# Performance work log

Hardware: AMD Instinct MI355X
Metric: run time of the kernel (lower is better)

## Reference

```python
import jax, jax.numpy as jnp
import numpy as np

MAX_LEN = 960
EMB = 200
SQRT_DK = np.sqrt(MAX_LEN).astype(np.float32)  # note: sqrt(max_len), as in source


def setup_inputs() -> dict:
    key = jax.random.key(0)
    k1, k2, k3, k4 = jax.random.split(key, 4)
    B, S, F = 16, 2048, 800
    x = jax.random.normal(k1, (B, S, F), dtype=jnp.float32)
    # torch Linear(960,200) weight init scale ~ 1/sqrt(960); random normal scaled
    scale = 1.0 / np.sqrt(MAX_LEN)
    Wq = jax.random.normal(k2, (MAX_LEN, EMB), dtype=jnp.float32) * scale
    Wk = jax.random.normal(k3, (MAX_LEN, EMB), dtype=jnp.float32) * scale
    Wv = jax.random.normal(k4, (MAX_LEN, EMB), dtype=jnp.float32) * scale
    return {"x": x, "Wq": Wq, "Wk": Wk, "Wv": Wv}


def reference(x, Wq, Wk, Wv):
    # pad feature dim up to MAX_LEN with zeros
    pad = MAX_LEN - x.shape[2]
    x = jnp.pad(x, ((0, 0), (0, 0), (0, pad)))
    gelu = lambda t: jax.nn.gelu(t, approximate=False)  # torch nn.GELU default = exact
    q = gelu(jnp.einsum('bsf,fe->bse', x, Wq))  # [B,S,E]
    k = gelu(jnp.einsum('bsf,fe->bse', x, Wk))
    v = gelu(jnp.einsum('bsf,fe->bse', x, Wv))
    score = jnp.einsum('bqe,bke->bqk', q, k) / SQRT_DK  # [B,S,S]
    attn = jax.nn.softmax(score, axis=-1)
    return jnp.einsum('bqk,bke->bqe', attn, v)  # [B,S,E]
```

## Files before the change

### kernel.cpp

```cpp
#include <hip/hip_runtime.h>
#include <hip/hip_bf16.h>

#define B_  16
#define S_  2048
#define F_  800
#define E_  200
#define EP  224
#define KP  832
#define KSP 256
#define M_  (B_ * S_)

typedef __attribute__((ext_vector_type(8))) short short8;
typedef __attribute__((ext_vector_type(4))) float f32x4;

#define QSCL (0.03227486121839514f * 1.4426950408889634f)

__device__ __forceinline__ unsigned short f2bf(float f) {
    __hip_bfloat16 h = __float2bfloat16(f);
    return *reinterpret_cast<unsigned short*>(&h);
}

__device__ __forceinline__ float exp2_fast(float x) {
    float r;
    asm("v_exp_f32 %0, %1" : "=v"(r) : "v"(x));
    return r;
}

__device__ __forceinline__ float rcp_fast(float x) {
    float r;
    asm("v_rcp_f32 %0, %1" : "=v"(r) : "v"(x));
    return r;
}

__device__ __forceinline__ float gelu_fast(float x) {
    const float i = x + 0.044715f * x * x * x;
    const float z = 2.302265314f * i;
    return x * rcp_fast(1.0f + exp2_fast(-z));
}

__device__ __forceinline__ void gload_lds16(const void* g, void* l) {
    __builtin_amdgcn_global_load_lds(
        (const __attribute__((address_space(1))) unsigned int*)g,
        (__attribute__((address_space(3))) unsigned int*)l, 16, 0, 0);
}

__global__ __launch_bounds__(256)
void prep_x(const float* __restrict__ x, unsigned short* __restrict__ xb) {
    const int id = blockIdx.x * 256 + threadIdx.x;
    const int r  = id / (KP / 8);
    const int c8 = id % (KP / 8);
    ushort4 lo = {0, 0, 0, 0}, hi = {0, 0, 0, 0};
    if (c8 < F_ / 8) {
        const float4 a = *reinterpret_cast<const float4*>(x + (size_t)r * F_ + c8 * 8);
        const float4 b = *reinterpret_cast<const float4*>(x + (size_t)r * F_ + c8 * 8 + 4);
        lo.x = f2bf(a.x); lo.y = f2bf(a.y); lo.z = f2bf(a.z); lo.w = f2bf(a.w);
        hi.x = f2bf(b.x); hi.y = f2bf(b.y); hi.z = f2bf(b.z); hi.w = f2bf(b.w);
    }
    unsigned short* dst = xb + (size_t)r * KP + c8 * 8;
    *reinterpret_cast<ushort4*>(dst) = lo;
    *reinterpret_cast<ushort4*>(dst + 4) = hi;
}

__global__ __launch_bounds__(256)
void prep_w(const float* __restrict__ Wq, const float* __restrict__ Wk,
            const float* __restrict__ Wv, unsigned short* __restrict__ wt) {
    const int id = blockIdx.x * 256 + threadIdx.x;
    const int sel = id / (EP * KP);
    const int rem = id % (EP * KP);
    const int e = rem / KP;
    const int k = rem % KP;
    const float* W = (sel == 0) ? Wq : ((sel == 1) ? Wk : Wv);
    float v = (e < E_ && k < F_) ? W[(size_t)k * E_ + e] : 0.0f;
    wt[id] = f2bf(v);
}

#define STAGE(XB, WB, KK) do {                                                   \
    const int k0s = (KK) * 32;                                                   \
    _Pragma("unroll")                                                            \
    for (int i = 0; i < 2; ++i) {                                                \
        const int j = w * 2 + i;                                                 \
        const int row = 16 * j + rS;                                             \
        gload_lds16(xb + (size_t)(m0 + row) * KP + k0s + ((pS ^ (row & 3)) * 8), \
                    &XB[j * 512]);                                               \
    }                                                                            \
    _Pragma("unroll")                                                            \
    for (int i = 0; i < 4; ++i) {                                                \
        const int j = i * 4 + w;                                                 \
        if (j < 14) {                                                            \
            const int row = 16 * j + rS;                                         \
            gload_lds16(wsel + (size_t)row * KP + k0s + ((pS ^ (row & 3)) * 8),  \
                        &WB[j * 512]);                                           \
        }                                                                        \
    }                                                                            \
} while (0)

#define COMPUTE(XB, WB) do {                                                     \
    short8 afr[4];                                                               \
    _Pragma("unroll")                                                            \
    for (int rf = 0; rf < 4; ++rf) {                                             \
        const int row = wr * 64 + rf * 16 + ln15;                                \
        afr[rf] = *reinterpret_cast<const short8*>(                              \
            &XB[row * 32 + ((g ^ (row & 3)) * 8)]);                              \
    }                                                                            \
    _Pragma("unroll")                                                            \
    for (int cf = 0; cf < 7; ++cf) {                                             \
        const int row = wc * 112 + cf * 16 + ln15;                               \
        short8 bfr = *reinterpret_cast<const short8*>(                           \
            &WB[row * 32 + ((g ^ (row & 3)) * 8)]);                              \
        _Pragma("unroll")                                                        \
        for (int rf = 0; rf < 4; ++rf)                                           \
            acc[rf][cf] = __builtin_amdgcn_mfma_f32_16x16x32_bf16(               \
                afr[rf], bfr, acc[rf][cf], 0, 0, 0);                             \
    }                                                                            \
} while (0)

__global__ __launch_bounds__(256, 2)
void gemm_qkv(const unsigned short* __restrict__ xb,
              const unsigned short* __restrict__ wt,
              unsigned short* __restrict__ qbuf,
              unsigned short* __restrict__ kbuf,
              unsigned short* __restrict__ vtbuf) {
    const int sel = blockIdx.y;
    const int m0 = blockIdx.x * 128;
    const int t = threadIdx.x;
    const int lane = t & 63;
    const int w = t >> 6;
    const int wr = w >> 1;
    const int wc = w & 1;
    const int ln15 = lane & 15;
    const int g = lane >> 4;

    __shared__ __align__(16) unsigned short X0s[128 * 32];
    __shared__ __align__(16) unsigned short W0s[224 * 32];
    __shared__ __align__(16) unsigned short X1s[128 * 32];
    __shared__ __align__(16) unsigned short W1s[224 * 32];

    const unsigned short* wsel = wt + (size_t)sel * EP * KP;

    f32x4 acc[4][7];
#pragma unroll
    for (int i = 0; i < 4; ++i)
#pragma unroll
        for (int j = 0; j < 7; ++j) acc[i][j] = (f32x4)0.0f;

    const int rS = lane >> 2;
    const int pS = lane & 3;

    STAGE(X0s, W0s, 0);
    __syncthreads();
#pragma unroll
    for (int p = 0; p < 12; ++p) {
        STAGE(X1s, W1s, 2 * p + 1);
        COMPUTE(X0s, W0s);
        __syncthreads();
        STAGE(X0s, W0s, 2 * p + 2);
        COMPUTE(X1s, W1s);
        __syncthreads();
    }
    STAGE(X1s, W1s, 25);
    COMPUTE(X0s, W0s);
    __syncthreads();
    COMPUTE(X1s, W1s);

#pragma unroll
    for (int rf = 0; rf < 4; ++rf) {
        const int row = m0 + wr * 64 + rf * 16 + g * 4;
#pragma unroll
        for (int cf = 0; cf < 7; ++cf) {
            const int col = wc * 112 + cf * 16 + ln15;
            if (sel == 0) {
#pragma unroll
                for (int tt = 0; tt < 4; ++tt)
                    qbuf[(size_t)(row + tt) * EP + col] =
                        f2bf(gelu_fast(acc[rf][cf][tt]) * QSCL);
            } else if (sel == 1) {
#pragma unroll
                for (int tt = 0; tt < 4; ++tt)
                    kbuf[(size_t)(row + tt) * KSP + col] = f2bf(gelu_fast(acc[rf][cf][tt]));
            } else {
                const int bb = row >> 11, s = row & 2047;
                ushort4 pk;
                if (col == 200) {
                    pk.x = 0x3F80; pk.y = 0x3F80; pk.z = 0x3F80; pk.w = 0x3F80;
                } else {
                    pk.x = f2bf(gelu_fast(acc[rf][cf][0]));
                    pk.y = f2bf(gelu_fast(acc[rf][cf][1]));
                    pk.z = f2bf(gelu_fast(acc[rf][cf][2]));
                    pk.w = f2bf(gelu_fast(acc[rf][cf][3]));
                }
                *reinterpret_cast<ushort4*>(
                    &vtbuf[((size_t)(bb * EP + col)) * S_ + s]) = pk;
            }
        }
    }
}

#define BQ  128
#define BKV 64

#define ASTAGE(KB, VB, KT) do {                                                  \
    const int kv0s = (KT) * BKV;                                                 \
    {                            \
        const int r_in = lane >> 5;                                              \
        const int p = lane & 31;                                                 \
        _Pragma("unroll")                                                        \
        for (int i = 0; i < 4; ++i) {                                            \
            const int j = w * 4 + i;                                             \
            const int row = 2 * j + r_in;                                        \
            gload_lds16(kb_b + (size_t)(kv0s + row) * KSP + ((p ^ ((row << 2) & 31)) * 8),\
                        &KB[j * 512]);                                           \
        }                                                                        \
    }                                                                            \
    {                                        \
        const int r_in = lane >> 3;                                              \
        const int p = lane & 7;                                                  \
        _Pragma("unroll")                                                        \
        for (int i = 0; i < 4; ++i) {                                            \
            const int j = i * 8 + w;                                             \
            if (j < 28) {                                                        \
                const int row = 8 * j + r_in;                                    \
                gload_lds16(vt_b + (size_t)row * S_ + kv0s + ((p ^ (row & 7)) * 8),\
                            &VB[j * 512]);                                       \
            }                                                                    \
        }                                                                        \
    }                                                                            \
} while (0)

#define ACOMPUTE(KB, VB) do {                                                    \
    f32x4 sacc[4];                                                               \
    __builtin_amdgcn_s_setprio(1);                                               \
    _Pragma("unroll")                                                            \
    for (int n = 0; n < 4; ++n) {                                                \
        f32x4 a = (f32x4)0.0f;                                                   \
        const int krow = n * 16 + ln15;                                          \
        const unsigned short* kr = &KB[krow * KSP];                              \
        const int rx = (krow << 2) & 31;                                         \
        _Pragma("unroll")                                                        \
        for (int s = 0; s < 7; ++s) {                                            \
            short8 bf = *reinterpret_cast<const short8*>(                        \
                kr + (((s * 4 + g) ^ rx) * 8));                                  \
            a = __builtin_amdgcn_mfma_f32_16x16x32_bf16(qf[s], bf, a, 0, 0, 0);  \
        }                                                                        \
        sacc[n] = a;                                                             \
    }                                                                            \
    __builtin_amdgcn_s_setprio(0);                                               \
    _Pragma("unroll")                                                            \
    for (int n = 0; n < 4; ++n)                                                  \
        _Pragma("unroll")                                                        \
        for (int tt = 0; tt < 4; ++tt)                                           \
            Plds[w][g * 4 + tt][n * 16 + ln15] = f2bf(exp2_fast(sacc[n][tt]));   \
    short8 pf0 = *reinterpret_cast<const short8*>(&Plds[w][ln15][g * 8]);        \
    short8 pf1 = *reinterpret_cast<const short8*>(&Plds[w][ln15][32 + g * 8]);   \
    __builtin_amdgcn_s_setprio(1);                                               \
    _Pragma("unroll")                                                            \
    for (int n = 0; n < 14; ++n) {                                               \
        const int vrow = n * 16 + ln15;                                          \
        const unsigned short* vr = &VB[vrow * 64];                               \
        const int rx = vrow & 7;                                                 \
        short8 b0 = *reinterpret_cast<const short8*>(vr + ((g ^ rx) * 8));       \
        short8 b1 = *reinterpret_cast<const short8*>(vr + (((4 + g) ^ rx) * 8)); \
        o[n] = __builtin_amdgcn_mfma_f32_16x16x32_bf16(pf0, b0, o[n], 0, 0, 0);  \
        o[n] = __builtin_amdgcn_mfma_f32_16x16x32_bf16(pf1, b1, o[n], 0, 0, 0);  \
    }                                                                            \
    __builtin_amdgcn_s_setprio(0);                                               \
} while (0)

__global__ __launch_bounds__(512, 2)
void attn_kernel(const unsigned short* __restrict__ qbuf,
                 const unsigned short* __restrict__ kbuf,
                 const unsigned short* __restrict__ vtbuf,
                 float* __restrict__ out) {
    const int id = blockIdx.x;
    const int slot = id >> 3;
    const int b = 2 * (id & 7) + (slot >> 4);
    const int q0 = (slot & 15) * BQ;
    const int t = threadIdx.x;
    const int lane = t & 63;
    const int w = t >> 6;
    const int ln15 = lane & 15;
    const int g = lane >> 4;

    __shared__ __align__(16) unsigned short Ks[2][BKV * KSP];
    __shared__ __align__(16) unsigned short Vts[2][EP * 64];
    __shared__ __align__(16) unsigned short Plds[8][16][68];

    short8 qf[7];
    {
        const unsigned short* qp =
            qbuf + (size_t)(b * S_ + q0 + w * 16 + ln15) * EP + g * 8;
#pragma unroll
        for (int s = 0; s < 7; ++s)
            qf[s] = *reinterpret_cast<const short8*>(qp + s * 32);
    }

    f32x4 o[14];
#pragma unroll
    for (int i = 0; i < 14; ++i) o[i] = (f32x4)0.0f;

    const unsigned short* kb_b = kbuf + (size_t)b * S_ * KSP;
    const unsigned short* vt_b = vtbuf + (size_t)b * EP * S_;

    ASTAGE(Ks[0], Vts[0], 0);
    __syncthreads();
    for (int kt = 0; kt < S_ / BKV - 1; ++kt) {
        const int cur = kt & 1;
        ASTAGE(Ks[cur ^ 1], Vts[cur ^ 1], kt + 1);
        ACOMPUTE(Ks[cur], Vts[cur]);
        __syncthreads();
    }
    ACOMPUTE(Ks[1], Vts[1]);

    {
        float l[4];
#pragma unroll
        for (int tt = 0; tt < 4; ++tt)
            l[tt] = __shfl(o[12][tt], (lane & 48) + 8, 64);
#pragma unroll
        for (int tt = 0; tt < 4; ++tt) {
            const float inv = 1.0f / l[tt];
            const int row = q0 + w * 16 + g * 4 + tt;
            float* op = out + (size_t)(b * S_ + row) * E_;
#pragma unroll
            for (int n = 0; n < 13; ++n) {
                const int e = n * 16 + ln15;
                if (e < E_) op[e] = o[n][tt] * inv;
            }
        }
    }
}

extern "C" void kernel_launch(void* const* d_in, const int* in_sizes, int n_in,
                              void* d_out, int out_size, void* d_ws, size_t ws_size,
                              hipStream_t stream) {
    const float* x  = (const float*)d_in[0];
    const float* Wq = (const float*)d_in[1];
    const float* Wk = (const float*)d_in[2];
    const float* Wv = (const float*)d_in[3];
    float* out = (float*)d_out;

    unsigned short* xb    = (unsigned short*)d_ws;
    unsigned short* wt    = xb + (size_t)M_ * KP;
    unsigned short* qbuf  = wt + (size_t)3 * EP * KP;
    unsigned short* kbuf  = qbuf + (size_t)M_ * EP;
    unsigned short* vtbuf = kbuf + (size_t)M_ * KSP;

    prep_x<<<dim3(M_ * (KP / 8) / 256), 256, 0, stream>>>(x, xb);
    prep_w<<<dim3(3 * EP * KP / 256), 256, 0, stream>>>(Wq, Wk, Wv, wt);
    gemm_qkv<<<dim3(256, 3), 256, 0, stream>>>(xb, wt, qbuf, kbuf, vtbuf);
    attn_kernel<<<dim3(256), 512, 0, stream>>>(qbuf, kbuf, vtbuf, out);
}
```

Baseline: 171.9 us.

## Fuse fp32-to-bf16 conversion of x into QKV GEMM staging

Removes the separate prep_x pass that wrote a padded bf16 copy of x, and instead loads fp32 x directly in the GEMM's staging step, converts it in registers and writes it to LDS. This drops a full read and write of the large bf16 intermediate plus one launch. The K loop is trimmed to 25 steps (800/32), so the zero-padded tail is no longer computed. In exchange, the X loads become synchronous register loads rather than async global-to-LDS copies, which may weaken overlap with the MFMA work, and x is read three times in fp32, once per Q/K/V grid slice.

```diff
diff --git a/kernel.cpp b/kernel.cpp
--- a/kernel.cpp
+++ b/kernel.cpp
@@ -42,23 +42,6 @@
     __builtin_amdgcn_global_load_lds(
         (const __attribute__((address_space(1))) unsigned int*)g,
         (__attribute__((address_space(3))) unsigned int*)l, 16, 0, 0);
-}
-
-__global__ __launch_bounds__(256)
-void prep_x(const float* __restrict__ x, unsigned short* __restrict__ xb) {
-    const int id = blockIdx.x * 256 + threadIdx.x;
-    const int r  = id / (KP / 8);
-    const int c8 = id % (KP / 8);
-    ushort4 lo = {0, 0, 0, 0}, hi = {0, 0, 0, 0};
-    if (c8 < F_ / 8) {
-        const float4 a = *reinterpret_cast<const float4*>(x + (size_t)r * F_ + c8 * 8);
-        const float4 b = *reinterpret_cast<const float4*>(x + (size_t)r * F_ + c8 * 8 + 4);
-        lo.x = f2bf(a.x); lo.y = f2bf(a.y); lo.z = f2bf(a.z); lo.w = f2bf(a.w);
-        hi.x = f2bf(b.x); hi.y = f2bf(b.y); hi.z = f2bf(b.z); hi.w = f2bf(b.w);
-    }
-    unsigned short* dst = xb + (size_t)r * KP + c8 * 8;
-    *reinterpret_cast<ushort4*>(dst) = lo;
-    *reinterpret_cast<ushort4*>(dst + 4) = hi;
 }
 
 __global__ __launch_bounds__(256)
@@ -74,15 +57,27 @@
     wt[id] = f2bf(v);
 }
 
-#define STAGE(XB, WB, KK) do {                                                   \
+#define STAGE_X(XB, KK) do {                                                     \
     const int k0s = (KK) * 32;                                                   \
     _Pragma("unroll")                                                            \
     for (int i = 0; i < 2; ++i) {                                                \
         const int j = w * 2 + i;                                                 \
         const int row = 16 * j + rS;                                             \
-        gload_lds16(xb + (size_t)(m0 + row) * KP + k0s + ((pS ^ (row & 3)) * 8), \
-                    &XB[j * 512]);                                               \
-    }                                                                            \
+        const float* xp = x + (size_t)(m0 + row) * F_ + k0s + pS * 8;            \
+        const float4 a = *reinterpret_cast<const float4*>(xp);                   \
+        const float4 bq = *reinterpret_cast<const float4*>(xp + 4);              \
+        union { unsigned short u[8]; short8 s; } pk;                             \
+        pk.u[0] = f2bf(a.x);  pk.u[1] = f2bf(a.y);                               \
+        pk.u[2] = f2bf(a.z);  pk.u[3] = f2bf(a.w);                               \
+        pk.u[4] = f2bf(bq.x); pk.u[5] = f2bf(bq.y);                              \
+        pk.u[6] = f2bf(bq.z); pk.u[7] = f2bf(bq.w);                              \
+        *reinterpret_cast<short8*>(                                              \
+            &XB[row * 32 + ((pS ^ (rS & 3)) * 8)]) = pk.s;                       \
+    }                                                                            \
+} while (0)
+
+#define STAGE_W(WB, KK) do {                                                     \
+    const int k0s = (KK) * 32;                                                   \
     _Pragma("unroll")                                                            \
     for (int i = 0; i < 4; ++i) {                                                \
         const int j = i * 4 + w;                                                 \
@@ -94,6 +89,8 @@
     }                                                                            \
 } while (0)
 
+#define STAGE(XB, WB, KK) do { STAGE_W(WB, KK); STAGE_X(XB, KK); } while (0)
+
 #define COMPUTE(XB, WB) do {                                                     \
     short8 afr[4];                                                               \
     _Pragma("unroll")                                                            \
@@ -115,7 +112,7 @@
 } while (0)
 
 __global__ __launch_bounds__(256, 2)
-void gemm_qkv(const unsigned short* __restrict__ xb,
+void gemm_qkv(const float* __restrict__ x,
               const unsigned short* __restrict__ wt,
               unsigned short* __restrict__ qbuf,
               unsigned short* __restrict__ kbuf,
@@ -157,10 +154,7 @@
         COMPUTE(X1s, W1s);
         __syncthreads();
     }
-    STAGE(X1s, W1s, 25);
     COMPUTE(X0s, W0s);
-    __syncthreads();
-    COMPUTE(X1s, W1s);
 
 #pragma unroll
     for (int rf = 0; rf < 4; ++rf) {
@@ -338,14 +332,12 @@
     const float* Wv = (const float*)d_in[3];
     float* out = (float*)d_out;
 
-    unsigned short* xb    = (unsigned short*)d_ws;
-    unsigned short* wt    = xb + (size_t)M_ * KP;
+    unsigned short* wt    = (unsigned short*)d_ws;
     unsigned short* qbuf  = wt + (size_t)3 * EP * KP;
     unsigned short* kbuf  = qbuf + (size_t)M_ * EP;
     unsigned short* vtbuf = kbuf + (size_t)M_ * KSP;
 
-    prep_x<<<dim3(M_ * (KP / 8) / 256), 256, 0, stream>>>(x, xb);
     prep_w<<<dim3(3 * EP * KP / 256), 256, 0, stream>>>(Wq, Wk, Wv, wt);
-    gemm_qkv<<<dim3(256, 3), 256, 0, stream>>>(xb, wt, qbuf, kbuf, vtbuf);
+    gemm_qkv<<<dim3(256, 3), 256, 0, stream>>>(x, wt, qbuf, kbuf, vtbuf);
     attn_kernel<<<dim3(256), 512, 0, stream>>>(qbuf, kbuf, vtbuf, out);
 }
```

Result: slower. 175.5 us (+2.1%).
